# Kernel tuning notes

Hardware: AMD Instinct MI355X
Metric: run time of the kernel (lower is better)

Reference implementation:

```python
import jax, jax.numpy as jnp
import numpy as np

M, N, DIM, B = 64, 64, 512, 4096
SIGMA = max(M, N) / 2.0  # default sigma in BaseSOM.__init__


def setup_inputs() -> dict:
    key = jax.random.key(0)
    k1, k2 = jax.random.split(key)
    batch = jax.random.normal(k1, (B, DIM), dtype=jnp.float32)
    weights = jax.random.uniform(k2, (M * N, DIM), dtype=jnp.float32)
    # grid locations [(i, j) for i in range(M) for j in range(N)]
    ii, jj = jnp.meshgrid(jnp.arange(M), jnp.arange(N), indexing="ij")
    locations = jnp.stack([ii.reshape(-1), jj.reshape(-1)], axis=1).astype(jnp.int64)
    return {
        "batch": batch,
        "weights": weights,
        "locations": locations,
        "decay_rate": 1000,
        "it": 100,
    }


def reference(batch, weights, locations, decay_rate, it):
    # Squared Euclidean distances (argmin is identical to argmin of cdist p=2).
    x2 = jnp.sum(batch * batch, axis=1, keepdims=True)          # [B, 1]
    w2 = jnp.sum(weights * weights, axis=1)[None, :]            # [1, MN]
    d2 = x2 - 2.0 * (batch @ weights.T) + w2                    # [B, MN]
    bmu_indices = jnp.argmin(d2, axis=1)                        # [B]
    bmu_loc = locations[bmu_indices]                            # [B, 2]
    lr = jnp.exp(-jnp.float32(it) / jnp.float32(decay_rate))
    sigma_op = jnp.float32(SIGMA) * lr
    # [B, MN, 2] grid offsets -> squared grid distance [B, MN]
    diff = locations[None, :, :].astype(jnp.float32) - bmu_loc[:, None, :].astype(jnp.float32)
    dist_sq = jnp.sum(diff * diff, axis=2)
    return jnp.exp(-dist_sq / (sigma_op * sigma_op))
```

## Files before the change

kernel.cpp:

```cpp
#include <hip/hip_runtime.h>
#include <cfloat>

#define DIMK 512
#define MN   4096
#define BATCH 4096
#define NGRP 1024

typedef _Float16 half8_t __attribute__((ext_vector_type(8)));
typedef _Float16 half4_t __attribute__((ext_vector_type(4)));
typedef float f32x4 __attribute__((ext_vector_type(4)));

#define GLD16(gp, lp) __builtin_amdgcn_global_load_lds( \
    (const __attribute__((address_space(1))) void*)(gp), \
    (__attribute__((address_space(3))) void*)(lp), 16, 0, 0)

__global__ __launch_bounds__(256) void convert_kernel(
        const float* __restrict__ X, const float* __restrict__ W,
        _Float16* __restrict__ Xh, _Float16* __restrict__ Wh,
        float* __restrict__ w2, float* __restrict__ xnorm) {
    const int blk  = blockIdx.x;
    const int t    = threadIdx.x;
    const bool isW = blk >= 1024;
    const float* src = isW ? W : X;
    _Float16* dst  = isW ? Wh : Xh;
    const int rblk = isW ? blk - 1024 : blk;
    const size_t idx = (size_t)rblk * 2048 + (size_t)t * 8;

    float4 v0 = *(const float4*)(src + idx);
    float4 v1 = *(const float4*)(src + idx + 4);
    float v[8] = {v0.x, v0.y, v0.z, v0.w, v1.x, v1.y, v1.z, v1.w};
    half8_t hv;
    float s = 0.f;
#pragma unroll
    for (int e = 0; e < 8; e++) {
        s += v[e] * v[e];
        hv[e] = (_Float16)v[e];
    }
    *(half8_t*)(dst + idx) = hv;
#pragma unroll
    for (int o = 32; o > 0; o >>= 1) s += __shfl_down(s, o);
    if ((t & 63) == 0) {
        int row = rblk * 4 + (t >> 6);
        if (isW) w2[row] = s;
        else     xnorm[row] = __fsqrt_rn(s);
    }
}

#define MFMA16(A0, A1, A2, A3, R) \
    do { \
        acc[(R)+0][0] = __builtin_amdgcn_mfma_f32_16x16x32_f16(A0, b0, acc[(R)+0][0], 0, 0, 0); \
        acc[(R)+0][1] = __builtin_amdgcn_mfma_f32_16x16x32_f16(A0, b1, acc[(R)+0][1], 0, 0, 0); \
        acc[(R)+0][2] = __builtin_amdgcn_mfma_f32_16x16x32_f16(A0, b2, acc[(R)+0][2], 0, 0, 0); \
        acc[(R)+0][3] = __builtin_amdgcn_mfma_f32_16x16x32_f16(A0, b3, acc[(R)+0][3], 0, 0, 0); \
        acc[(R)+1][0] = __builtin_amdgcn_mfma_f32_16x16x32_f16(A1, b0, acc[(R)+1][0], 0, 0, 0); \
        acc[(R)+1][1] = __builtin_amdgcn_mfma_f32_16x16x32_f16(A1, b1, acc[(R)+1][1], 0, 0, 0); \
        acc[(R)+1][2] = __builtin_amdgcn_mfma_f32_16x16x32_f16(A1, b2, acc[(R)+1][2], 0, 0, 0); \
        acc[(R)+1][3] = __builtin_amdgcn_mfma_f32_16x16x32_f16(A1, b3, acc[(R)+1][3], 0, 0, 0); \
        acc[(R)+2][0] = __builtin_amdgcn_mfma_f32_16x16x32_f16(A2, b0, acc[(R)+2][0], 0, 0, 0); \
        acc[(R)+2][1] = __builtin_amdgcn_mfma_f32_16x16x32_f16(A2, b1, acc[(R)+2][1], 0, 0, 0); \
        acc[(R)+2][2] = __builtin_amdgcn_mfma_f32_16x16x32_f16(A2, b2, acc[(R)+2][2], 0, 0, 0); \
        acc[(R)+2][3] = __builtin_amdgcn_mfma_f32_16x16x32_f16(A2, b3, acc[(R)+2][3], 0, 0, 0); \
        acc[(R)+3][0] = __builtin_amdgcn_mfma_f32_16x16x32_f16(A3, b0, acc[(R)+3][0], 0, 0, 0); \
        acc[(R)+3][1] = __builtin_amdgcn_mfma_f32_16x16x32_f16(A3, b1, acc[(R)+3][1], 0, 0, 0); \
        acc[(R)+3][2] = __builtin_amdgcn_mfma_f32_16x16x32_f16(A3, b2, acc[(R)+3][2], 0, 0, 0); \
        acc[(R)+3][3] = __builtin_amdgcn_mfma_f32_16x16x32_f16(A3, b3, acc[(R)+3][3], 0, 0, 0); \
    } while (0)

__global__ __launch_bounds__(512, 2) void score_kernel(
        const _Float16* __restrict__ Xh, const _Float16* __restrict__ Wh,
        const float* __restrict__ w2, float* __restrict__ Gm ) {
    __shared__ __align__(16) _Float16 lds[4][2][8192];

    const int t    = threadIdx.x;
    const int lane = t & 63;
    const int w    = t >> 6;
    const int wm   = w >> 2;
    const int wn   = w & 3;

    const int id  = blockIdx.y * 16 + blockIdx.x;
    const int xcd = id & 7;
    const int li  = id >> 3;
    const int bm  = (xcd >> 1) * 4 + (li >> 3);
    const int bn  = (xcd & 1) * 8 + (li & 7);
    const int m0  = bm * 256;
    const int n0  = bn * 256;

    const int srow = (t >> 6) * 16 + (t & 15);
    const int skof = ((t >> 4) & 3) * 8;
    const _Float16* gA = Xh + (size_t)(m0 + srow) * DIMK + skof;
    const _Float16* gB = Wh + (size_t)(n0 + srow) * DIMK + skof;
    const int ldst = t * 8;

#define STG_A(bf, kt, c) GLD16(gA + (size_t)(c) * (128 * DIMK) + (kt) * 32, &lds[bf][0][(c) * 4096 + ldst])
#define STG_B(bf, kt, c) GLD16(gB + (size_t)(c) * (128 * DIMK) + (kt) * 32, &lds[bf][1][(c) * 4096 + ldst])
#define LDA(bf, rg) (*(const half8_t*)(&lds[bf][0][(rg) * 512 + lane * 8]))
#define LDB(bf, rg) (*(const half8_t*)(&lds[bf][1][(rg) * 512 + lane * 8]))

    f32x4 acc[8][4];
#pragma unroll
    for (int i = 0; i < 8; i++)
#pragma unroll
        for (int j = 0; j < 4; j++) acc[i][j] = (f32x4){0.f, 0.f, 0.f, 0.f};

    STG_A(0, 0, 0); STG_A(0, 0, 1); STG_B(0, 0, 0); STG_B(0, 0, 1);
    STG_A(1, 1, 0); STG_A(1, 1, 1); STG_B(1, 1, 0); STG_B(1, 1, 1);
    STG_A(2, 2, 0); STG_A(2, 2, 1); STG_B(2, 2, 0); STG_B(2, 2, 1);

#pragma unroll
    for (int kt = 0; kt < 16; ++kt) {
        const int bf = kt & 3;
        const int nb = (kt + 3) & 3;

        if (kt <= 13)      { asm volatile("s_waitcnt vmcnt(8)" ::: "memory"); }
        else if (kt == 14) { asm volatile("s_waitcnt vmcnt(4)" ::: "memory"); }
        else               { asm volatile("s_waitcnt vmcnt(0)" ::: "memory"); }
        __builtin_amdgcn_sched_barrier(0);
        __builtin_amdgcn_s_barrier();

        if (kt <= 12) { STG_A(nb, kt + 3, 0); STG_A(nb, kt + 3, 1); }

        half8_t a0 = LDA(bf, wm * 8 + 0), a1 = LDA(bf, wm * 8 + 1);
        half8_t a2 = LDA(bf, wm * 8 + 2), a3 = LDA(bf, wm * 8 + 3);
        half8_t b0 = LDB(bf, wn * 4 + 0), b1 = LDB(bf, wn * 4 + 1);
        half8_t b2 = LDB(bf, wn * 4 + 2), b3 = LDB(bf, wn * 4 + 3);
        half8_t a4 = LDA(bf, wm * 8 + 4), a5 = LDA(bf, wm * 8 + 5);
        half8_t a6 = LDA(bf, wm * 8 + 6), a7 = LDA(bf, wm * 8 + 7);

        if (kt <= 12) { STG_B(nb, kt + 3, 0); STG_B(nb, kt + 3, 1); }

        asm volatile("s_waitcnt lgkmcnt(4)" ::: "memory");
        __builtin_amdgcn_sched_barrier(0);
        __builtin_amdgcn_s_setprio(1);
        MFMA16(a0, a1, a2, a3, 0);
        __builtin_amdgcn_s_setprio(0);

        asm volatile("s_waitcnt lgkmcnt(0)" ::: "memory");
        __builtin_amdgcn_sched_barrier(0);
        __builtin_amdgcn_s_setprio(1);
        MFMA16(a4, a5, a6, a7, 4);
        __builtin_amdgcn_s_setprio(0);
    }

    const int q   = lane >> 4;
    const int cl  = lane & 15;
    const int gb  = (n0 >> 2) + wn * 16;
    float w2v[4];
#pragma unroll
    for (int j = 0; j < 4; j++) w2v[j] = w2[n0 + wn * 64 + j * 16 + cl];
#pragma unroll
    for (int ai = 0; ai < 8; ai++)
#pragma unroll
        for (int v = 0; v < 4; v++) {
            const int row = m0 + wm * 128 + ai * 16 + q * 4 + v;
            _Float16* grow = (_Float16*)Gm + (size_t)row * 8192 + gb;
#pragma unroll
            for (int j = 0; j < 4; j++) {
                float s = w2v[j] - 2.0f * acc[ai][j][v];
                s = fminf(s, __shfl_xor(s, 1));
                s = fminf(s, __shfl_xor(s, 2));
                if ((cl & 3) == 0) grow[j * 4 + (cl >> 2)] = (_Float16)s;
            }
        }
}

__global__ __launch_bounds__(256) void epilogue_kernel(
        const float* __restrict__ w2, const float* __restrict__ xnorm,
        const float* __restrict__ X, const float* __restrict__ W,
        const int* __restrict__ decay_p, const int* __restrict__ it_p,
        float* out) {
    __shared__ float xs[512];
    __shared__ int   list[NGRP];
    __shared__ int   cnt;
    __shared__ float wmin[4];
    __shared__ float svv[4];
    __shared__ int   svi[4];
    __shared__ float tab[128];
    const int row  = blockIdx.x;
    const int t    = threadIdx.x;
    const int lane = t & 63;
    const int w    = t >> 6;

    {
        float2 xv = *(const float2*)(X + (size_t)row * DIMK + t * 2);
        xs[2 * t]     = xv.x;
        xs[2 * t + 1] = xv.y;
    }
    if (t == 0) cnt = 0;

    half4_t gmh = *((const half4_t*)((const _Float16*)out + (size_t)row * 8192) + t);
    float gme[4] = {(float)gmh[0], (float)gmh[1], (float)gmh[2], (float)gmh[3]};
    float g = fminf(fminf(gme[0], gme[1]), fminf(gme[2], gme[3]));
#pragma unroll
    for (int mask = 1; mask <= 32; mask <<= 1)
        g = fminf(g, __shfl_xor(g, mask));
    if (lane == 0) wmin[w] = g;
    __syncthreads();
    const float gmin = fminf(fminf(wmin[0], wmin[1]), fminf(wmin[2], wmin[3]));
    const float tau  = gmin + 2.0f * (0.0222f * xnorm[row] + 0.25f);

#pragma unroll
    for (int e = 0; e < 4; e++)
        if (gme[e] <= tau) list[atomicAdd(&cnt, 1)] = t * 4 + e;
    __syncthreads();
    const int total = cnt;

    float mbv = FLT_MAX;
    int   mbi = 0x7FFFFFFF;
    for (int idx = w; idx < total; idx += 4) {
        const int gid = list[idx];
#pragma unroll
        for (int cj = 0; cj < 4; cj++) {
            const int col = gid * 4 + cj;
            const float* wr = W + (size_t)col * DIMK;
            float p = 0.f;
#pragma unroll
            for (int e = 0; e < 8; e++) p += xs[lane * 8 + e] * wr[lane * 8 + e];
#pragma unroll
            for (int mask = 1; mask <= 32; mask <<= 1) p += __shfl_xor(p, mask);
            float s = w2[col] - 2.0f * p;
            if (s < mbv || (s == mbv && col < mbi)) { mbv = s; mbi = col; }
        }
    }
    if (lane == 0) { svv[w] = mbv; svi[w] = mbi; }
    __syncthreads();
    float sbv = svv[0]; int sbi = svi[0];
#pragma unroll
    for (int k = 1; k < 4; k++) {
        float s = svv[k]; int c = svi[k];
        if (s < sbv || (s == sbv && c < sbi)) { sbv = s; sbi = c; }
    }

    const float lr  = __expf(-(float)(*it_p) / (float)(*decay_p));
    const float so  = 32.0f * lr;
    const float inv = 1.0f / (so * so);
    const int rr = sbi >> 6, cc = sbi & 63;
    if (t < 64) {
        float d = (float)(t - rr);
        tab[t] = __expf(-d * d * inv);
    } else if (t < 128) {
        float d = (float)(t - 64 - cc);
        tab[t] = __expf(-d * d * inv);
    }
    __syncthreads();
    const float* er = tab;
    const float* ec = tab + 64;
    f32x4* orow = (f32x4*)(out + (size_t)row * 4096);
#pragma unroll
    for (int qq = 0; qq < 4; qq++) {
        int f  = qq * 256 + t;
        int i  = f >> 4;
        int j0 = (f & 15) * 4;
        float e = er[i];
        f32x4 o = {e * ec[j0], e * ec[j0 + 1], e * ec[j0 + 2], e * ec[j0 + 3]};
        __builtin_nontemporal_store(o, orow + f);
    }
}

extern "C" void kernel_launch(void* const* d_in, const int* in_sizes, int n_in,
                              void* d_out, int out_size, void* d_ws, size_t ws_size,
                              hipStream_t stream) {
    const float* X       = (const float*)d_in[0];
    const float* W       = (const float*)d_in[1];
    const int*   decay_p = (const int*)d_in[3];
    const int*   it_p    = (const int*)d_in[4];
    float* out = (float*)d_out;

    _Float16* Xh = (_Float16*)d_ws;
    _Float16* Wh = Xh + (size_t)BATCH * DIMK;
    float*    w2 = (float*)(Wh + (size_t)MN * DIMK);
    float*    xn = w2 + MN;

    convert_kernel<<<2048, 256, 0, stream>>>(X, W, Xh, Wh, w2, xn);
    score_kernel<<<dim3(16, 16), 512, 0, stream>>>(Xh, Wh, w2, out);
    epilogue_kernel<<<BATCH, 256, 0, stream>>>(w2, xn, X, W, decay_p, it_p, out);
}
```

Before: 135.5 us.

## Split epilogue into argmin and gauss kernels with compact fp16 score buffer

Group-min scores now go to a dense workspace buffer (row stride 1024 halves) instead of being packed into the output with a stride of 8192, which shrinks their footprint and improves locality. The epilogue is split into an argmin kernel and a separate gaussian-writing kernel, so the heavy output store no longer shares a kernel with the refinement's W-row gathers. The refinement now has each 16-lane group handle one column with float4 loads and packs (score, index) into 64-bit keys for the min reduction. This costs an extra kernel launch and a small bmu round-trip through global memory.

Result: no change. 137.0 us (+1.1%).

```diff
diff --git a/kernel.cpp b/kernel.cpp
--- a/kernel.cpp
+++ b/kernel.cpp
@@ -68,7 +68,7 @@
 
 __global__ __launch_bounds__(512, 2) void score_kernel(
         const _Float16* __restrict__ Xh, const _Float16* __restrict__ Wh,
-        const float* __restrict__ w2, float* __restrict__ Gm ) {
+        const float* __restrict__ w2, _Float16* __restrict__ Gm) {
     __shared__ __align__(16) _Float16 lds[4][2][8192];
 
     const int t    = threadIdx.x;
@@ -152,7 +152,7 @@
 #pragma unroll
         for (int v = 0; v < 4; v++) {
             const int row = m0 + wm * 128 + ai * 16 + q * 4 + v;
-            _Float16* grow = (_Float16*)Gm + (size_t)row * 8192 + gb;
+            _Float16* grow = Gm + (size_t)row * 1024 + gb;
 #pragma unroll
             for (int j = 0; j < 4; j++) {
                 float s = w2v[j] - 2.0f * acc[ai][j][v];
@@ -163,18 +163,15 @@
         }
 }
 
-__global__ __launch_bounds__(256) void epilogue_kernel(
+__global__ __launch_bounds__(256) void argmin_kernel(
         const float* __restrict__ w2, const float* __restrict__ xnorm,
         const float* __restrict__ X, const float* __restrict__ W,
-        const int* __restrict__ decay_p, const int* __restrict__ it_p,
-        float* out) {
+        const _Float16* __restrict__ gm, int* __restrict__ bmu) {
     __shared__ float xs[512];
     __shared__ int   list[NGRP];
     __shared__ int   cnt;
     __shared__ float wmin[4];
-    __shared__ float svv[4];
-    __shared__ int   svi[4];
-    __shared__ float tab[128];
+    __shared__ unsigned long long wkey[4];
     const int row  = blockIdx.x;
     const int t    = threadIdx.x;
     const int lane = t & 63;
@@ -187,7 +184,7 @@
     }
     if (t == 0) cnt = 0;
 
-    half4_t gmh = *((const half4_t*)((const _Float16*)out + (size_t)row * 8192) + t);
+    half4_t gmh = *((const half4_t*)(gm + (size_t)row * 1024) + t);
     float gme[4] = {(float)gmh[0], (float)gmh[1], (float)gmh[2], (float)gmh[3]};
     float g = fminf(fminf(gme[0], gme[1]), fminf(gme[2], gme[3]));
 #pragma unroll
@@ -204,31 +201,53 @@
     __syncthreads();
     const int total = cnt;
 
-    float mbv = FLT_MAX;
-    int   mbi = 0x7FFFFFFF;
+    const int s16 = lane & 15;
+    const int cg  = lane >> 4;
+    float4 xq[8];
+#pragma unroll
+    for (int e = 0; e < 8; e++) xq[e] = ((const float4*)xs)[e * 16 + s16];
+
+    unsigned long long mkey = ~0ULL;
     for (int idx = w; idx < total; idx += 4) {
-        const int gid = list[idx];
-#pragma unroll
-        for (int cj = 0; cj < 4; cj++) {
-            const int col = gid * 4 + cj;
-            const float* wr = W + (size_t)col * DIMK;
-            float p = 0.f;
-#pragma unroll
-            for (int e = 0; e < 8; e++) p += xs[lane * 8 + e] * wr[lane * 8 + e];
-#pragma unroll
-            for (int mask = 1; mask <= 32; mask <<= 1) p += __shfl_xor(p, mask);
-            float s = w2[col] - 2.0f * p;
-            if (s < mbv || (s == mbv && col < mbi)) { mbv = s; mbi = col; }
+        const int col = list[idx] * 4 + cg;
+        const float4* wr = (const float4*)(W + (size_t)col * DIMK);
+        float p = 0.f;
+#pragma unroll
+        for (int e = 0; e < 8; e++) {
+            float4 wv = wr[e * 16 + s16];
+            p += xq[e].x * wv.x + xq[e].y * wv.y
+               + xq[e].z * wv.z + xq[e].w * wv.w;
         }
-    }
-    if (lane == 0) { svv[w] = mbv; svi[w] = mbi; }
-    __syncthreads();
-    float sbv = svv[0]; int sbi = svi[0];
-#pragma unroll
-    for (int k = 1; k < 4; k++) {
-        float s = svv[k]; int c = svi[k];
-        if (s < sbv || (s == sbv && c < sbi)) { sbv = s; sbi = c; }
-    }
+        p += __shfl_xor(p, 1); p += __shfl_xor(p, 2);
+        p += __shfl_xor(p, 4); p += __shfl_xor(p, 8);
+        const float s = w2[col] - 2.0f * p;
+        unsigned int b = __float_as_uint(s);
+        unsigned int u = (b & 0x80000000u) ? ~b : (b | 0x80000000u);
+        unsigned long long key = ((unsigned long long)u << 32) | (unsigned int)col;
+        mkey = key < mkey ? key : mkey;
+    }
+    {
+        unsigned long long o;
+        o = __shfl_xor(mkey, 16); mkey = o < mkey ? o : mkey;
+        o = __shfl_xor(mkey, 32); mkey = o < mkey ? o : mkey;
+    }
+    if (lane == 0) wkey[w] = mkey;
+    __syncthreads();
+    if (t == 0) {
+        unsigned long long k = wkey[0];
+#pragma unroll
+        for (int i = 1; i < 4; i++) k = wkey[i] < k ? wkey[i] : k;
+        bmu[row] = (int)(k & 0xffffffffu);
+    }
+}
+
+__global__ __launch_bounds__(256) void gauss_kernel(
+        const int* __restrict__ bmu, const int* __restrict__ decay_p,
+        const int* __restrict__ it_p, float* __restrict__ out) {
+    __shared__ float tab[128];
+    const int row = blockIdx.x;
+    const int t   = threadIdx.x;
+    const int sbi = bmu[row];
 
     const float lr  = __expf(-(float)(*it_p) / (float)(*decay_p));
     const float so  = 32.0f * lr;
@@ -269,8 +288,11 @@
     _Float16* Wh = Xh + (size_t)BATCH * DIMK;
     float*    w2 = (float*)(Wh + (size_t)MN * DIMK);
     float*    xn = w2 + MN;
+    _Float16* gmv = (_Float16*)(xn + BATCH);
+    int*      bmu = (int*)(gmv + (size_t)BATCH * 1024);
 
     convert_kernel<<<2048, 256, 0, stream>>>(X, W, Xh, Wh, w2, xn);
-    score_kernel<<<dim3(16, 16), 512, 0, stream>>>(Xh, Wh, w2, out);
-    epilogue_kernel<<<BATCH, 256, 0, stream>>>(w2, xn, X, W, decay_p, it_p, out);
-}
+    score_kernel<<<dim3(16, 16), 512, 0, stream>>>(Xh, Wh, w2, gmv);
+    argmin_kernel<<<BATCH, 256, 0, stream>>>(w2, xn, X, W, gmv, bmu);
+    gauss_kernel<<<BATCH, 256, 0, stream>>>(bmu, decay_p, it_p, out);
+}
```
